# Kernel tuning notes

Measured on AMD Instinct MI355X. Metric: run time of the kernel, lower is better.

## Reference

```python
import jax, jax.numpy as jnp
import numpy as np

N = 50000          # number of nodes / output rows (len(degs))
IN_C, OUT_C = 16, 16
EDGE_F = 13        # edge feature dim fed to filter net
HID = 32           # filter-net hidden width
E_NOMINAL = 800000 # target number of edges (sum of degs)


def setup_inputs() -> dict:
    rng = np.random.default_rng(0)
    # variable per-node degrees in [0, 32], adjusted so they sum exactly to E_NOMINAL
    degs = rng.integers(0, 33, size=N).astype(np.int64)
    degs[0] = max(0, degs[0] + (E_NOMINAL - int(degs.sum())))
    E = int(degs.sum())
    # segment id of each edge = destination node (equivalent to the degs-driven loop)
    idxd = np.repeat(np.arange(N, dtype=np.int32), degs)
    idxn = rng.integers(0, N, size=E).astype(np.int32)  # source node gather index

    key = jax.random.key(0)
    k1, k2, k3, k4 = jax.random.split(key, 4)
    x = jax.random.normal(k1, (N, IN_C), jnp.float32)
    edgefeats = jax.random.normal(k2, (E, EDGE_F), jnp.float32)
    # filter net: Linear(EDGE_F->HID) -> ReLU -> Linear(HID->IN_C*OUT_C)
    W1 = jax.random.normal(k3, (EDGE_F, HID), jnp.float32) / np.float32(np.sqrt(EDGE_F))
    b1 = jnp.zeros((HID,), jnp.float32)
    W2 = jax.random.normal(k4, (HID, IN_C * OUT_C), jnp.float32) / np.float32(np.sqrt(HID))
    b2 = jnp.zeros((IN_C * OUT_C,), jnp.float32)
    return {
        "x": x, "edgefeats": edgefeats,
        "W1": W1, "b1": b1, "W2": W2, "b2": b2,
        "idxn": jnp.asarray(idxn), "idxd": jnp.asarray(idxd),
        "degs": jnp.asarray(degs.astype(np.float32)),
    }


def reference(x, edgefeats, W1, b1, W2, b2, idxn, idxd, degs):
    # filter net generates a per-edge [IN_C, OUT_C] weight matrix
    h = jax.nn.relu(edgefeats @ W1 + b1)                 # [E, HID]
    w = (h @ W2 + b2).reshape(-1, IN_C, OUT_C)           # [E, IN_C, OUT_C]
    # gather source-node features and apply per-edge matvec (bmm with [E,1,IN_C])
    sel = x[idxn]                                        # [E, IN_C]
    prod = jnp.einsum('ei,eio->eo', sel, w)              # [E, OUT_C]
    # segment-mean over each node's incoming edges; degree-0 nodes -> 0
    s = jax.ops.segment_sum(prod, idxd, num_segments=N)  # [N, OUT_C]
    d = degs[:, None]
    return jnp.where(d > 0, s / jnp.maximum(d, 1.0), jnp.float32(0.0))
```

## Files before the change

kernel.cpp:

```cpp
#include <hip/hip_runtime.h>

typedef _Float16 half2v __attribute__((ext_vector_type(2)));
typedef _Float16 half4v __attribute__((ext_vector_type(4)));
typedef _Float16 half8v __attribute__((ext_vector_type(8)));
typedef float   float4v __attribute__((ext_vector_type(4)));

#define INC     16
#define OUTC    16
#define EFN     13
#define HIDC    32
#define EPW     128
#define WPB     4
#define MAXSPAN 40

#define GLOBAL_AS __attribute__((address_space(1)))
#define LDS_AS    __attribute__((address_space(3)))

union H8 { half8v v; half2v h2[4]; };

__global__ __launch_bounds__(256) void prep(
    const float* __restrict__ W2,
    const float* __restrict__ x,
    _Float16*    __restrict__ wsB,
    _Float16*    __restrict__ wsXh,
    int nh)
{
    const int b = blockIdx.x;
    if (b < 32) {
        const int i = b * 256 + threadIdx.x;
        const int j = i & 7;
        const int l = (i >> 3) & 63;
        const int t = i >> 9;
        const int q = l >> 4, n = l & 15;
        const int kk = (j < 4) ? (q * 4 + j) : (16 + q * 4 + (j & 3));
        wsB[i] = (_Float16)W2[kk * 256 + t * 16 + n];
    } else {
        const int i = (b - 32) * 256 + threadIdx.x;
        if (i * 8 < nh) {
            const float4 v0 = ((const float4*)x)[i * 2];
            const float4 v1 = ((const float4*)x)[i * 2 + 1];
            half8v h;
            h[0] = (_Float16)v0.x; h[1] = (_Float16)v0.y;
            h[2] = (_Float16)v0.z; h[3] = (_Float16)v0.w;
            h[4] = (_Float16)v1.x; h[5] = (_Float16)v1.y;
            h[6] = (_Float16)v1.z; h[7] = (_Float16)v1.w;
            *(half8v*)(wsXh + (size_t)i * 8) = h;
        }
    }
}

__global__ __launch_bounds__(256, 4) void edge_kernel(
    const _Float16* __restrict__ xh,
    const float* __restrict__ edgefeats,
    const float* __restrict__ W1,
    const float* __restrict__ b1,
    const float* __restrict__ b2,
    const int*   __restrict__ idxn,
    const int*   __restrict__ idxd,
    const float* __restrict__ degs,
    const _Float16* __restrict__ wsB,
    float*       __restrict__ out,
    float*       __restrict__ wsPfirst,
    float*       __restrict__ wsPlast,
    int*         __restrict__ wsMeta,
    int E)
{
    __shared__ __align__(16) float sEF[WPB][EPW * EFN];
    __shared__ __align__(16) int   sidxn[WPB][EPW];
    __shared__ float lacc[WPB][MAXSPAN * OUTC];

    const int tid  = threadIdx.x;
    const int lane = tid & 63;
    const int wid  = tid >> 6;
    const int n    = lane & 15;
    const int q    = lane >> 4;

    const long vw = (long)blockIdx.x * WPB + wid;
    const long b0 = vw * EPW;
    if (b0 >= (long)E) return;
    const long bEnd = (b0 + EPW < (long)E) ? (b0 + EPW) : (long)E;
    const bool full = (b0 + EPW <= (long)E);
    const long Em1  = (long)E - 1;

    float* sEF_w   = sEF[wid];
    int*   sidxn_w = sidxn[wid];
    float* lacc_w  = lacc[wid];

    const long ea = b0 + n, eb = b0 + 16 + n;
    const int nd0 = idxn[(ea <= Em1) ? ea : Em1];
    const int nd1 = idxn[(eb <= Em1) ? eb : Em1];
    __builtin_amdgcn_sched_barrier(0);

    if (full) {
        const char* efsrc = (const char*)edgefeats + (size_t)b0 * (EFN * 4);
        #pragma unroll
        for (int c = 0; c < 6; ++c)
            __builtin_amdgcn_global_load_lds(
                (const GLOBAL_AS unsigned int*)(efsrc + c * 1024 + lane * 16),
                (LDS_AS unsigned int*)((char*)sEF_w + c * 1024), 16, 0, 0);
        if (lane < 32) {
            __builtin_amdgcn_global_load_lds(
                (const GLOBAL_AS unsigned int*)(efsrc + 6144 + lane * 16),
                (LDS_AS unsigned int*)((char*)sEF_w + 6144), 16, 0, 0);
            __builtin_amdgcn_global_load_lds(
                (const GLOBAL_AS unsigned int*)((const char*)(idxn + b0) + lane * 16),
                (LDS_AS unsigned int*)sidxn_w, 16, 0, 0);
        }
    } else {
        const long mx = (long)E * EFN - 1;
        for (int i = lane; i < EPW * EFN; i += 64) {
            long gi = b0 * EFN + i;
            if (gi > mx) gi = mx;
            sEF_w[i] = edgefeats[gi];
        }
        for (int i = lane; i < EPW; i += 64) {
            long e = b0 + i;
            if (e > Em1) e = Em1;
            sidxn_w[i] = idxn[e];
        }
    }
    __builtin_amdgcn_sched_barrier(0);

    const int d_lo = idxd[b0];
    const int d_hi = idxd[bEnd - 1];
    const int span = d_hi - d_lo;

    H8 bfr[16];
    #pragma unroll
    for (int t = 0; t < 16; ++t)
        bfr[t].v = *(const half8v*)(wsB + ((size_t)(t * 64 + lane) * 8));

    #pragma unroll
    for (int it = 0; it < MAXSPAN * OUTC / 64; ++it) lacc_w[lane + it * 64] = 0.0f;

    half4v a1, a2;
    float4v c1, c2;
    #pragma unroll
    for (int jj = 0; jj < 4; ++jj) {
        const int f = q * 4 + jj;
        const bool ok = (f < EFN);
        a1[jj] = ok ? (_Float16)W1[f * HIDC + n]      : (_Float16)0.f;
        a2[jj] = ok ? (_Float16)W1[f * HIDC + 16 + n] : (_Float16)0.f;
        c1[jj] = b1[q * 4 + jj];
        c2[jj] = b1[16 + q * 4 + jj];
    }
    half8v bfragB2;
    #pragma unroll
    for (int j = 0; j < 8; ++j) {
        _Float16 val = (_Float16)0.f;
        if (q < 2) val = (_Float16)b2[(q * 8 + j) * 16 + n];
        bfragB2[j] = val;
    }

    const int f0i = (q < 3) ? (q * 4) : 9;

    half8v pxa0 = *(const half8v*)(xh + (size_t)nd0 * INC);
    half8v pxb0 = *(const half8v*)(xh + (size_t)nd0 * INC + 8);
    half8v pxa1 = *(const half8v*)(xh + (size_t)nd1 * INC);
    half8v pxb1 = *(const half8v*)(xh + (size_t)nd1 * INC + 8);
    __builtin_amdgcn_sched_barrier(0);

    asm volatile("s_waitcnt vmcnt(0) lgkmcnt(0)" ::: "memory");
    __builtin_amdgcn_sched_barrier(0);

    #pragma unroll
    for (int t16 = 0; t16 < 8; ++t16) {
        const long base = b0 + (long)t16 * 16;
        const bool vM   = (base + n < (long)E);

        const half8v xA = (t16 & 1) ? pxa1 : pxa0;
        const half8v xB = (t16 & 1) ? pxb1 : pxb0;
        if (t16 < 6) {
            const int ndn = sidxn_w[(t16 + 2) * 16 + n];
            if (t16 & 1) {
                pxa1 = *(const half8v*)(xh + (size_t)ndn * INC);
                pxb1 = *(const half8v*)(xh + (size_t)ndn * INC + 8);
            } else {
                pxa0 = *(const half8v*)(xh + (size_t)ndn * INC);
                pxb0 = *(const half8v*)(xh + (size_t)ndn * INC + 8);
            }
        }
        long de = base + q * 4;
        if (de > (long)E - 4) de = (long)E - 4;
        const int4 dd = *(const int4*)(idxd + de);
        __builtin_amdgcn_sched_barrier(0);

        const float* efp = sEF_w + (size_t)(t16 * 16 + n) * EFN + f0i;
        const float e0 = efp[0], e1 = efp[1], e2 = efp[2], e3 = efp[3];

        H8 sa, sb_;
        sa.v = xA; sb_.v = xB;
        const half2v zz = {(_Float16)0.f, (_Float16)0.f};
        half2v selh[8];
        #pragma unroll
        for (int i = 0; i < 4; ++i) {
            selh[i]     = vM ? sa.h2[i]  : zz;
            selh[4 + i] = vM ? sb_.h2[i] : zz;
        }

        half4v efB;
        if (q < 3) {
            efB[0] = (_Float16)e0; efB[1] = (_Float16)e1;
            efB[2] = (_Float16)e2; efB[3] = (_Float16)e3;
        } else {
            efB[0] = (_Float16)e3; efB[1] = (_Float16)0.f;
            efB[2] = (_Float16)0.f; efB[3] = (_Float16)0.f;
        }

        const float4v hf1 = __builtin_amdgcn_mfma_f32_16x16x16f16(a1, efB, c1, 0, 0, 0);
        const float4v hf2 = __builtin_amdgcn_mfma_f32_16x16x16f16(a2, efB, c2, 0, 0, 0);

        H8 hu;
        #pragma unroll
        for (int r = 0; r < 2; ++r) {
            half2v t1 = {(_Float16)fmaxf(hf1[2*r], 0.f), (_Float16)fmaxf(hf1[2*r+1], 0.f)};
            half2v t2 = {(_Float16)fmaxf(hf2[2*r], 0.f), (_Float16)fmaxf(hf2[2*r+1], 0.f)};
            hu.h2[r]     = t1;
            hu.h2[2 + r] = t2;
        }

        float4v acc = {0.f, 0.f, 0.f, 0.f};
        #pragma unroll
        for (int t = 0; t < 16; ++t) {
            _Float16 sv = (t & 1) ? selh[t >> 1][1] : selh[t >> 1][0];
            half2v sb = {sv, sv};
            H8 a;
            a.h2[0] = sb * hu.h2[0];
            a.h2[1] = sb * hu.h2[1];
            a.h2[2] = sb * hu.h2[2];
            a.h2[3] = sb * hu.h2[3];
            acc = __builtin_amdgcn_mfma_f32_16x16x32_f16(a.v, bfr[t].v, acc, 0, 0, 0);
        }
        {
            H8 a;
            #pragma unroll
            for (int j2 = 0; j2 < 4; ++j2) {
                a.h2[j2] = (q < 2) ? selh[q * 4 + j2] : zz;
            }
            acc = __builtin_amdgcn_mfma_f32_16x16x32_f16(a.v, bfragB2, acc, 0, 0, 0);
        }

        const int r0 = ((dd.x < d_hi) ? dd.x : d_hi) - d_lo;
        const int r1 = ((dd.y < d_hi) ? dd.y : d_hi) - d_lo;
        const int r2 = ((dd.z < d_hi) ? dd.z : d_hi) - d_lo;
        const int r3 = ((dd.w < d_hi) ? dd.w : d_hi) - d_lo;
        if (r0 == r3) {
            atomicAdd(&lacc_w[r0 * OUTC + n], acc[0] + acc[1] + acc[2] + acc[3]);
        } else {
            atomicAdd(&lacc_w[r0 * OUTC + n], acc[0]);
            atomicAdd(&lacc_w[r1 * OUTC + n], acc[1]);
            atomicAdd(&lacc_w[r2 * OUTC + n], acc[2]);
            atomicAdd(&lacc_w[r3 * OUTC + n], acc[3]);
        }
    }

    asm volatile("s_waitcnt lgkmcnt(0)" ::: "memory");

    const bool first_starts = (b0 == 0)        || (idxd[b0 - 1] != d_lo);
    const bool last_ends    = (bEnd == (long)E) || (idxd[bEnd]   != d_hi);

    for (int i = lane; i < (span + 1) * OUTC; i += 64) {
        const int u = i >> 4;
        const int o = i & 15;
        const int v = d_lo + u;
        const float bin = lacc_w[u * OUTC + o];
        const bool starts = (u > 0)    || first_starts;
        const bool ends   = (u < span) || last_ends;
        if (starts && ends) {
            const float dg = degs[v];
            out[(size_t)v * OUTC + o] = (dg > 0.0f) ? bin / dg : 0.0f;
        } else if (!starts) {
            wsPfirst[(size_t)vw * OUTC + o] = bin;
        } else {
            wsPlast[(size_t)vw * OUTC + o] = bin;
        }
    }
    if (lane == 0) {
        wsMeta[vw * 4 + 0] = d_hi;
        wsMeta[vw * 4 + 1] = last_ends ? 1 : 0;
        wsMeta[vw * 4 + 2] =
            (((span > 0) || first_starts) && !last_ends) ? 1 : 0;
    }
}

__global__ __launch_bounds__(256) void fixup_kernel(
    const float* __restrict__ degs,
    float*       __restrict__ out,
    const float* __restrict__ wsPfirst,
    const float* __restrict__ wsPlast,
    const int*   __restrict__ wsMeta,
    int N, int nvw)
{
    const int t = blockIdx.x * 256 + threadIdx.x;

    if (t < nvw && wsMeta[t * 4 + 2]) {
        const int v = wsMeta[t * 4 + 0];
        float tot[OUTC];
        #pragma unroll
        for (int o = 0; o < OUTC; ++o) tot[o] = wsPlast[(size_t)t * OUTC + o];
        for (int j = t + 1; j < nvw; ++j) {
            #pragma unroll
            for (int o = 0; o < OUTC; ++o) tot[o] += wsPfirst[(size_t)j * OUTC + o];
            if (wsMeta[j * 4 + 0] != v || wsMeta[j * 4 + 1]) break;
        }
        const float dg = degs[v];
        #pragma unroll
        for (int o = 0; o < OUTC; ++o) out[(size_t)v * OUTC + o] = tot[o] / dg;
    }

    if (t < N && degs[t] == 0.0f) {
        float4* op = (float4*)(out + (size_t)t * OUTC);
        const float4 z = make_float4(0, 0, 0, 0);
        op[0] = z; op[1] = z; op[2] = z; op[3] = z;
    }
}

extern "C" void kernel_launch(void* const* d_in, const int* in_sizes, int n_in,
                              void* d_out, int out_size, void* d_ws, size_t ws_size,
                              hipStream_t stream)
{
    const float* x         = (const float*)d_in[0];
    const float* edgefeats = (const float*)d_in[1];
    const float* W1        = (const float*)d_in[2];
    const float* b1        = (const float*)d_in[3];
    const float* W2        = (const float*)d_in[4];
    const float* b2        = (const float*)d_in[5];
    const int*   idxn      = (const int*)d_in[6];
    const int*   idxd      = (const int*)d_in[7];
    const float* degs      = (const float*)d_in[8];

    const int E = in_sizes[6];
    const int N = in_sizes[8];
    const int nvw   = (E + EPW - 1) / EPW;
    const int gridw = (nvw + WPB - 1) / WPB;
    const int nh = N * INC;

    _Float16* wsB  = (_Float16*)d_ws;
    _Float16* wsXh = (_Float16*)((char*)d_ws + 16384);
    size_t xh_bytes = ((size_t)nh * 2 + 255) & ~(size_t)255;
    float* wsPfirst = (float*)((char*)d_ws + 16384 + xh_bytes);
    float* wsPlast  = wsPfirst + (size_t)nvw * OUTC;
    int*   wsMeta   = (int*)(wsPlast + (size_t)nvw * OUTC);

    const int xhblocks = (nh / 8 + 255) / 256;
    prep<<<32 + xhblocks, 256, 0, stream>>>(W2, x, wsB, wsXh, nh);

    edge_kernel<<<gridw, 256, 0, stream>>>(wsXh, edgefeats, W1, b1, b2,
                                           idxn, idxd, degs, wsB, (float*)d_out,
                                           wsPfirst, wsPlast, wsMeta, E);

    const int fthreads = (N > nvw) ? N : nvw;
    fixup_kernel<<<(fthreads + 255) / 256, 256, 0, stream>>>(
        degs, (float*)d_out, wsPfirst, wsPlast, wsMeta, N, nvw);
}
```

Before: 193.0 us.

## Replace cross-wave fixup kernel with global atomics on boundary segments

```diff
diff --git a/kernel.cpp b/kernel.cpp
--- a/kernel.cpp
+++ b/kernel.cpp
@@ -23,6 +23,7 @@
     const float* __restrict__ x,
     _Float16*    __restrict__ wsB,
     _Float16*    __restrict__ wsXh,
+    float*       __restrict__ out,
     int nh)
 {
     const int b = blockIdx.x;
@@ -36,6 +37,8 @@
         wsB[i] = (_Float16)W2[kk * 256 + t * 16 + n];
     } else {
         const int i = (b - 32) * 256 + threadIdx.x;
+        if (i * 4 < nh)
+            ((float4*)out)[i] = make_float4(0, 0, 0, 0);
         if (i * 8 < nh) {
             const float4 v0 = ((const float4*)x)[i * 2];
             const float4 v1 = ((const float4*)x)[i * 2 + 1];
@@ -49,7 +52,7 @@
     }
 }
 
-__global__ __launch_bounds__(256, 4) void edge_kernel(
+__global__ __launch_bounds__(256, 3) void edge_kernel(
     const _Float16* __restrict__ xh,
     const float* __restrict__ edgefeats,
     const float* __restrict__ W1,
@@ -60,9 +63,6 @@
     const float* __restrict__ degs,
     const _Float16* __restrict__ wsB,
     float*       __restrict__ out,
-    float*       __restrict__ wsPfirst,
-    float*       __restrict__ wsPlast,
-    int*         __restrict__ wsMeta,
     int E)
 {
     __shared__ __align__(16) float sEF[WPB][EPW * EFN];
@@ -266,52 +266,13 @@
         const float bin = lacc_w[u * OUTC + o];
         const bool starts = (u > 0)    || first_starts;
         const bool ends   = (u < span) || last_ends;
+        const float dg = degs[v];
+        const float val = (dg > 0.0f) ? bin / dg : 0.0f;
         if (starts && ends) {
-            const float dg = degs[v];
-            out[(size_t)v * OUTC + o] = (dg > 0.0f) ? bin / dg : 0.0f;
-        } else if (!starts) {
-            wsPfirst[(size_t)vw * OUTC + o] = bin;
+            out[(size_t)v * OUTC + o] = val;
         } else {
-            wsPlast[(size_t)vw * OUTC + o] = bin;
-        }
-    }
-    if (lane == 0) {
-        wsMeta[vw * 4 + 0] = d_hi;
-        wsMeta[vw * 4 + 1] = last_ends ? 1 : 0;
-        wsMeta[vw * 4 + 2] =
-            (((span > 0) || first_starts) && !last_ends) ? 1 : 0;
-    }
-}
-
-__global__ __launch_bounds__(256) void fixup_kernel(
-    const float* __restrict__ degs,
-    float*       __restrict__ out,
-    const float* __restrict__ wsPfirst,
-    const float* __restrict__ wsPlast,
-    const int*   __restrict__ wsMeta,
-    int N, int nvw)
-{
-    const int t = blockIdx.x * 256 + threadIdx.x;
-
-    if (t < nvw && wsMeta[t * 4 + 2]) {
-        const int v = wsMeta[t * 4 + 0];
-        float tot[OUTC];
-        #pragma unroll
-        for (int o = 0; o < OUTC; ++o) tot[o] = wsPlast[(size_t)t * OUTC + o];
-        for (int j = t + 1; j < nvw; ++j) {
-            #pragma unroll
-            for (int o = 0; o < OUTC; ++o) tot[o] += wsPfirst[(size_t)j * OUTC + o];
-            if (wsMeta[j * 4 + 0] != v || wsMeta[j * 4 + 1]) break;
-        }
-        const float dg = degs[v];
-        #pragma unroll
-        for (int o = 0; o < OUTC; ++o) out[(size_t)v * OUTC + o] = tot[o] / dg;
-    }
-
-    if (t < N && degs[t] == 0.0f) {
-        float4* op = (float4*)(out + (size_t)t * OUTC);
-        const float4 z = make_float4(0, 0, 0, 0);
-        op[0] = z; op[1] = z; op[2] = z; op[3] = z;
+            atomicAdd(&out[(size_t)v * OUTC + o], val);
+        }
     }
 }
 
@@ -337,19 +298,11 @@
 
     _Float16* wsB  = (_Float16*)d_ws;
     _Float16* wsXh = (_Float16*)((char*)d_ws + 16384);
-    size_t xh_bytes = ((size_t)nh * 2 + 255) & ~(size_t)255;
-    float* wsPfirst = (float*)((char*)d_ws + 16384 + xh_bytes);
-    float* wsPlast  = wsPfirst + (size_t)nvw * OUTC;
-    int*   wsMeta   = (int*)(wsPlast + (size_t)nvw * OUTC);
-
-    const int xhblocks = (nh / 8 + 255) / 256;
-    prep<<<32 + xhblocks, 256, 0, stream>>>(W2, x, wsB, wsXh, nh);
+
+    const int zblocks = (nh / 4 + 255) / 256;
+    prep<<<32 + zblocks, 256, 0, stream>>>(W2, x, wsB, wsXh, (float*)d_out, nh);
 
     edge_kernel<<<gridw, 256, 0, stream>>>(wsXh, edgefeats, W1, b1, b2,
-                                           idxn, idxd, degs, wsB, (float*)d_out,
-                                           wsPfirst, wsPlast, wsMeta, E);
-
-    const int fthreads = (N > nvw) ? N : nvw;
-    fixup_kernel<<<(fthreads + 255) / 256, 256, 0, stream>>>(
-        degs, (float*)d_out, wsPfirst, wsPlast, wsMeta, N, nvw);
+                                           idxn, idxd, degs, wsB,
+                                           (float*)d_out, E);
 }
```

New measurement: 158.1 us. 1.22x faster.
